# Kernel optimization log

Hardware: AMD Instinct MI355X
Metric: run time of the kernel (lower is better)

The kernel has to match this reference:

```python
import jax, jax.numpy as jnp
import numpy as np

N = 50000      # batch_num_nodes
E = 800000     # num edges (~avg degree 16)
A = 16         # num_atom_types
H = 64         # hidden dim
Z = 32         # latent dim
L_ENC = 2
L_DEC = 2
C_NORM = 16.0  # coordinate-update normalization (avg degree)


def _glorot(key, shape):
    fan = shape[-2] + shape[-1]
    return jax.random.normal(key, shape, dtype=jnp.float32) * np.float32(np.sqrt(2.0 / fan))


def _make_stack(key, n_layers, h_dim):
    # Stacked per-layer EGNN params: edge MLP (2 layers), coord head, node MLP (2 layers).
    def one(k):
        k0, k1, k2, k3, k4 = jax.random.split(k, 5)
        return (_glorot(k0, (2 * h_dim + 1, h_dim)), jnp.zeros((h_dim,), jnp.float32),
                _glorot(k1, (h_dim, h_dim)), jnp.zeros((h_dim,), jnp.float32),
                _glorot(k2, (h_dim, 1)),
                _glorot(k3, (2 * h_dim, h_dim)), jnp.zeros((h_dim,), jnp.float32),
                _glorot(k4, (h_dim, h_dim)), jnp.zeros((h_dim,), jnp.float32))
    parts = [one(k) for k in jax.random.split(key, n_layers)]
    return tuple(jnp.stack(p) for p in zip(*parts))


PARAM_NAMES = ["We1", "be1", "We2", "be2", "Wx", "Wn1", "bn1", "Wn2", "bn2"]


def setup_inputs() -> dict:
    key = jax.random.key(0)
    k = jax.random.split(key, 10)
    h = jax.random.normal(k[0], (N, A), dtype=jnp.float32)
    x = jax.random.normal(k[1], (N, 3), dtype=jnp.float32)
    edge_index = jax.random.randint(k[2], (2, E), 0, N, dtype=jnp.int32)
    inp = {"h": h, "x": x, "edge_index": edge_index,
           "W_emb": _glorot(k[3], (A, H)), "b_emb": jnp.zeros((H,), jnp.float32),
           "W_lat": _glorot(k[4], (H, Z)), "b_lat": jnp.zeros((Z,), jnp.float32),
           "W_up": _glorot(k[5], (Z, H)), "b_up": jnp.zeros((H,), jnp.float32),
           "W_out": _glorot(k[6], (H, A)), "b_out": jnp.zeros((A,), jnp.float32)}
    for n, p in zip(PARAM_NAMES, _make_stack(k[7], L_ENC, H)):
        inp["enc_" + n] = p
    for n, p in zip(PARAM_NAMES, _make_stack(k[8], L_DEC, H)):
        inp["dec_" + n] = p
    return inp


def _egnn_layer(h, x, src, dst, We1, be1, We2, be2, Wx, Wn1, bn1, Wn2, bn2):
    rel = x[src] - x[dst]                                    # [E, 3] gather
    d2 = jnp.sum(rel * rel, axis=-1, keepdims=True)          # [E, 1]
    ef = jnp.concatenate([h[src], h[dst], d2], axis=-1)      # [E, 2H+1]
    m = jax.nn.silu(jax.nn.silu(ef @ We1 + be1) @ We2 + be2)  # [E, H] per-edge message
    # equivariant coordinate update: scatter-add weighted relative vectors
    x = x + jax.ops.segment_sum(rel * (m @ Wx), dst, num_segments=N) / C_NORM
    agg = jnp.asarray(jax.ops.segment_sum(m, dst, num_segments=N))  # [N, H]
    h = h + jax.nn.silu(jnp.concatenate([h, agg], axis=-1) @ Wn1 + bn1) @ Wn2 + bn2
    return h, x


def reference(h, x, edge_index, W_emb, b_emb, W_lat, b_lat, W_up, b_up, W_out, b_out,
              enc_We1, enc_be1, enc_We2, enc_be2, enc_Wx, enc_Wn1, enc_bn1, enc_Wn2, enc_bn2,
              dec_We1, dec_be1, dec_We2, dec_be2, dec_Wx, dec_Wn1, dec_bn1, dec_Wn2, dec_bn2):
    src, dst = edge_index[0], edge_index[1]
    hh = h @ W_emb + b_emb
    for i in range(L_ENC):
        hh, x = _egnn_layer(hh, x, src, dst,
                            enc_We1[i], enc_be1[i], enc_We2[i], enc_be2[i], enc_Wx[i],
                            enc_Wn1[i], enc_bn1[i], enc_Wn2[i], enc_bn2[i])
    z = hh @ W_lat + b_lat                                   # latent [N, Z]
    hh = z @ W_up + b_up
    for i in range(L_DEC):
        hh, x = _egnn_layer(hh, x, src, dst,
                            dec_We1[i], dec_be1[i], dec_We2[i], dec_be2[i], dec_Wx[i],
                            dec_Wn1[i], dec_bn1[i], dec_Wn2[i], dec_bn2[i])
    h_rec = hh @ W_out + b_out                               # reconstructed atom-type logits
    return jnp.concatenate([h_rec, x], axis=-1)              # [N, A+3]
```

## Files before the change

kernel.cpp:

```cpp
#include <hip/hip_runtime.h>

#define NN 50000
#define NE 800000
#define MAXC 100000
#define EBLK 2048
#define SCB ((NN + 255) / 256)

__device__ __forceinline__ float silu_f(float v) {
    return v * __builtin_amdgcn_rcpf(1.f + __expf(-v));
}

typedef __bf16 bf16;
typedef bf16 v8bf __attribute__((ext_vector_type(8)));
typedef float v4f __attribute__((ext_vector_type(4)));

#define UNPACK8(dstv, ptr) { \
    float4 _a = reinterpret_cast<const float4*>(ptr)[0]; \
    float4 _b = reinterpret_cast<const float4*>(ptr)[1]; \
    dstv[0]=_a.x; dstv[1]=_a.y; dstv[2]=_a.z; dstv[3]=_a.w; \
    dstv[4]=_b.x; dstv[5]=_b.y; dstv[6]=_b.z; dstv[7]=_b.w; }

__global__ __launch_bounds__(256) void k_embed(
    const float* __restrict__ h_in, const float* __restrict__ x_in,
    const float* __restrict__ W, const float* __restrict__ b,
    float* __restrict__ h, float* __restrict__ xp)
{
    int t = blockIdx.x * 256 + threadIdx.x;
    if (t < NN * 4) { int n = t >> 2, c = t & 3; xp[t] = (c < 3) ? x_in[n * 3 + c] : 0.f; }
    int n = t >> 6, j = t & 63;
    const float* hr = h_in + n * 16;
    float acc = b[j];
#pragma unroll
    for (int k = 0; k < 16; k++) acc = fmaf(hr[k], W[k * 64 + j], acc);
    h[t] = acc;
}

__global__ __launch_bounds__(256) void k_prep_all(
    const float* __restrict__ eW1, const float* __restrict__ dW1,
    const float* __restrict__ eW2, const float* __restrict__ dW2,
    const float* __restrict__ eN1, const float* __restrict__ dN1,
    const float* __restrict__ eN2, const float* __restrict__ dN2,
    bf16* __restrict__ We1h, bf16* __restrict__ We1l,
    bf16* __restrict__ We2h, bf16* __restrict__ We2l,
    bf16* __restrict__ Wn1h, bf16* __restrict__ Wn1l,
    bf16* __restrict__ Wn2h, bf16* __restrict__ Wn2l)
{
    int t = blockIdx.x * 256 + threadIdx.x;
    const float *encW, *decW; int K, stride; bf16 *Wh, *Wl; int r;
    if (t < 32768)      { r = t;         encW = eW1; decW = dW1; K = 128; stride = 129 * 64; Wh = We1h; Wl = We1l; }
    else if (t < 49152) { r = t - 32768; encW = eW2; decW = dW2; K = 64;  stride = 64 * 64;  Wh = We2h; Wl = We2l; }
    else if (t < 81920) { r = t - 49152; encW = eN1; decW = dN1; K = 128; stride = 128 * 64; Wh = Wn1h; Wl = Wn1l; }
    else                { r = t - 81920; encW = eN2; decW = dN2; K = 64;  stride = 64 * 64;  Wh = Wn2h; Wl = Wn2l; }
    int per = K * 64;
    int li = r / per, rr = r - li * per;
    int k = rr >> 6, col = rr & 63;
    const float* Wsrc = (li < 2 ? encW : decW) + (li & 1) * stride;
    float w = Wsrc[k * 64 + col];
    bf16 hi = (bf16)w;
    int kh = k >> 5, gg = (k >> 3) & 3, b = k & 7;
    int di = li * per + (((kh * 4 + gg) * 64 + col) * 8 + b);
    Wh[di] = hi; Wl[di] = (bf16)(w - (float)hi);
}

__global__ __launch_bounds__(256) void k_zero_cnt(int* __restrict__ cnt)
{
    int t = blockIdx.x * 256 + threadIdx.x;
    if (t <= NN) cnt[t] = 0;
}

__global__ __launch_bounds__(256) void k_hist(const int* __restrict__ dst, int* __restrict__ cnt)
{
    int e = blockIdx.x * 256 + threadIdx.x;
    if (e < NE) atomicAdd(&cnt[dst[e]], 1);
}

__global__ __launch_bounds__(256) void k_blocksum(
    const int* __restrict__ cnt, int* __restrict__ bsum)
{
    int b = blockIdx.x, tid = threadIdx.x;
    int i = b * 256 + tid;
    int deg = (i < NN) ? cnt[i] : 0;
    int chk = (deg + 15) >> 4;
#pragma unroll
    for (int d = 1; d < 64; d <<= 1) { deg += __shfl_xor(deg, d); chk += __shfl_xor(chk, d); }
    __shared__ int sd[4], sc[4];
    int wv = tid >> 6;
    if ((tid & 63) == 0) { sd[wv] = deg; sc[wv] = chk; }
    __syncthreads();
    if (tid == 0) {
        bsum[b] = sd[0] + sd[1] + sd[2] + sd[3];
        bsum[SCB + b] = sc[0] + sc[1] + sc[2] + sc[3];
    }
}

__global__ __launch_bounds__(256) void k_scanbase(
    const int* __restrict__ bsum, int* __restrict__ bbase, int* __restrict__ ncptr)
{
    __shared__ int s[256], s2[256];
    int tid = threadIdx.x;
    int v  = (tid < SCB) ? bsum[tid] : 0;
    int v2 = (tid < SCB) ? bsum[SCB + tid] : 0;
    s[tid] = v; s2[tid] = v2;
    __syncthreads();
    for (int d = 1; d < 256; d <<= 1) {
        int u  = (tid >= d) ? s[tid - d] : 0;
        int u2 = (tid >= d) ? s2[tid - d] : 0;
        __syncthreads();
        s[tid] += u; s2[tid] += u2;
        __syncthreads();
    }
    if (tid < SCB) {
        bbase[tid]       = s[tid] - v;
        bbase[SCB + tid] = s2[tid] - v2;
    }
    if (tid == 255) *ncptr = s2[SCB - 1];
}

__global__ __launch_bounds__(256) void k_applyscan(
    int* __restrict__ cnt , const int* __restrict__ bbase,
    int* __restrict__ off, int* __restrict__ cur, int* __restrict__ coff)
{
    int b = blockIdx.x, tid = threadIdx.x;
    int i = b * 256 + tid;
    int deg = (i < NN) ? cnt[i] : 0;
    int chk = (deg + 15) >> 4;
    __shared__ int s[256], s2[256];
    s[tid] = deg; s2[tid] = chk;
    __syncthreads();
    for (int d = 1; d < 256; d <<= 1) {
        int u  = (tid >= d) ? s[tid - d] : 0;
        int u2 = (tid >= d) ? s2[tid - d] : 0;
        __syncthreads();
        s[tid] += u; s2[tid] += u2;
        __syncthreads();
    }
    if (i < NN) {
        int o = bbase[b] + s[tid] - deg;
        off[i] = o; cur[i] = o;
        coff[i] = bbase[SCB + b] + s2[tid] - chk;
    }
    if (i == 0) off[NN] = NE;
}

__global__ __launch_bounds__(256) void k_chunkfill(
    const int* __restrict__ off, const int* __restrict__ coff, int2* __restrict__ cpair)
{
    int n = blockIdx.x * 256 + threadIdx.x;
    if (n >= NN) return;
    int b = off[n], e = off[n + 1], co = coff[n];
    int single = ((e - b) <= 16) ? (1 << 25) : 0;
    for (int eb = b; eb < e; eb += 16) {
        int cnt = min(e - eb, 16);
        cpair[co++] = make_int2(n, eb | (cnt << 20) | single);
    }
}

__global__ __launch_bounds__(256) void k_scatter(
    const int* __restrict__ dst, const int* __restrict__ srcArr,
    int* __restrict__ cur, int* __restrict__ srcp)
{
    int e = blockIdx.x * 256 + threadIdx.x;
    if (e < NE) { int p = atomicAdd(&cur[dst[e]], 1); srcp[p] = srcArr[e]; }
}

__global__ __launch_bounds__(256) void k_pq_mfma(
    const float* __restrict__ h,
    const bf16* __restrict__ We1h, const bf16* __restrict__ We1l,
    const float* __restrict__ be1,
    float* __restrict__ P, float* __restrict__ Q,
    float* __restrict__ agg, float* __restrict__ dxb)
{
    const int wv = threadIdx.x >> 6, lane = threadIdx.x & 63;
    const int g = lane >> 4, l15 = lane & 15;
    const int n0 = (blockIdx.x * 4 + wv) * 16;
    if (n0 >= NN) return;
    const int nrow = n0 + l15;

    v8bf Ah[2], Al[2];
#pragma unroll
    for (int kh = 0; kh < 2; kh++) {
        float v[8];
        UNPACK8(v, h + nrow * 64 + kh * 32 + g * 8);
#pragma unroll
        for (int b = 0; b < 8; b++) {
            bf16 hi = (bf16)v[b];
            Ah[kh][b] = hi; Al[kh][b] = (bf16)(v[b] - (float)hi);
        }
    }

    const v8bf* Bh = reinterpret_cast<const v8bf*>(We1h);
    const v8bf* Bl = reinterpret_cast<const v8bf*>(We1l);

    float be1v[4];
#pragma unroll
    for (int nt = 0; nt < 4; nt++) be1v[nt] = be1[l15 + 16 * nt];

#pragma unroll
    for (int nt = 0; nt < 4; nt++) {
        v4f ap = {0.f,0.f,0.f,0.f}, aq = {0.f,0.f,0.f,0.f};
#pragma unroll
        for (int kh = 0; kh < 2; kh++) {
            int fiP = (kh * 4 + g) * 64 + l15 + 16 * nt;
            int fiQ = ((kh + 2) * 4 + g) * 64 + l15 + 16 * nt;
            v8bf bph = Bh[fiP], bpl = Bl[fiP];
            v8bf bqh = Bh[fiQ], bql = Bl[fiQ];
            ap = __builtin_amdgcn_mfma_f32_16x16x32_bf16(Ah[kh], bph, ap, 0, 0, 0);
            ap = __builtin_amdgcn_mfma_f32_16x16x32_bf16(Ah[kh], bpl, ap, 0, 0, 0);
            ap = __builtin_amdgcn_mfma_f32_16x16x32_bf16(Al[kh], bph, ap, 0, 0, 0);
            aq = __builtin_amdgcn_mfma_f32_16x16x32_bf16(Ah[kh], bqh, aq, 0, 0, 0);
            aq = __builtin_amdgcn_mfma_f32_16x16x32_bf16(Ah[kh], bql, aq, 0, 0, 0);
            aq = __builtin_amdgcn_mfma_f32_16x16x32_bf16(Al[kh], bqh, aq, 0, 0, 0);
        }
#pragma unroll
        for (int i = 0; i < 4; i++) {
            int ro = (n0 + g * 4 + i) * 64 + l15 + 16 * nt;
            P[ro] = ap[i] + be1v[nt];
            Q[ro] = aq[i];
            agg[ro] = 0.f;
        }
    }
    {
        int nd = lane >> 2, cc = lane & 3;
        if (cc < 3) dxb[(n0 + nd) * 3 + cc] = 0.f;
    }
}

__device__ __forceinline__ void edge_compute(
    int n, int ct, int sg,
    const float4& xn, const float4& xs,
    const float4* pw, const float4* qv4,
    const v8bf* __restrict__ BHf, const v8bf* __restrict__ BLf,
    const float (&wdv)[2][8], const float (&be2v)[4], const float (&wxv)[4],
    int g, int l15, int lane,
    float* __restrict__ agg, float* __restrict__ dxb)
{
    float rx = xs.x - xn.x, ry = xs.y - xn.y, rz = xs.z - xn.z;
    float d2 = rx * rx + ry * ry + rz * rz;
    const float* pv = reinterpret_cast<const float*>(pw);
    const float* qv = reinterpret_cast<const float*>(qv4);

    v8bf Ah[2], Al[2];
#pragma unroll
    for (int kh = 0; kh < 2; kh++) {
#pragma unroll
        for (int b = 0; b < 8; b++) {
            float m1 = silu_f(pv[kh * 8 + b] + qv[kh * 8 + b] + d2 * wdv[kh][b]);
            bf16 hi = (bf16)m1;
            Ah[kh][b] = hi;
            Al[kh][b] = (bf16)(m1 - (float)hi);
        }
    }

    v4f acc[4];
#pragma unroll
    for (int nt = 0; nt < 4; nt++) {
        v4f a = {0.f, 0.f, 0.f, 0.f};
#pragma unroll
        for (int kh = 0; kh < 2; kh++) {
            int fi = (kh * 4 + g) * 64 + l15 + 16 * nt;
            v8bf bh = BHf[fi], bl = BLf[fi];
            a = __builtin_amdgcn_mfma_f32_16x16x32_bf16(Ah[kh], bh, a, 0, 0, 0);
            a = __builtin_amdgcn_mfma_f32_16x16x32_bf16(Ah[kh], bl, a, 0, 0, 0);
            a = __builtin_amdgcn_mfma_f32_16x16x32_bf16(Al[kh], bh, a, 0, 0, 0);
        }
        acc[nt] = a;
    }

    float aggv[4] = {0.f, 0.f, 0.f, 0.f};
    float dxx = 0.f, dxy = 0.f, dxz = 0.f;
#pragma unroll
    for (int i = 0; i < 4; i++) {
        bool valid = (g * 4 + i) < ct;
        float m0 = silu_f(acc[0][i] + be2v[0]); m0 = valid ? m0 : 0.f;
        float m1 = silu_f(acc[1][i] + be2v[1]); m1 = valid ? m1 : 0.f;
        float m2 = silu_f(acc[2][i] + be2v[2]); m2 = valid ? m2 : 0.f;
        float m3 = silu_f(acc[3][i] + be2v[3]); m3 = valid ? m3 : 0.f;
        aggv[0] += m0; aggv[1] += m1; aggv[2] += m2; aggv[3] += m3;
        float pd = m0 * wxv[0] + m1 * wxv[1] + m2 * wxv[2] + m3 * wxv[3];
        pd += __shfl_xor(pd, 1); pd += __shfl_xor(pd, 2);
        pd += __shfl_xor(pd, 4); pd += __shfl_xor(pd, 8);
        float rxe = __shfl(rx, g * 4 + i);
        float rye = __shfl(ry, g * 4 + i);
        float rze = __shfl(rz, g * 4 + i);
        if (l15 == 0) { dxx += rxe * pd; dxy += rye * pd; dxz += rze * pd; }
    }

#pragma unroll
    for (int nt = 0; nt < 4; nt++) {
        aggv[nt] += __shfl_xor(aggv[nt], 16);
        aggv[nt] += __shfl_xor(aggv[nt], 32);
    }
    if (lane < 16) {
        if (sg) {
#pragma unroll
            for (int nt = 0; nt < 4; nt++) agg[n * 64 + l15 + 16 * nt] = aggv[nt];
        } else {
#pragma unroll
            for (int nt = 0; nt < 4; nt++) unsafeAtomicAdd(&agg[n * 64 + l15 + 16 * nt], aggv[nt]);
        }
    }
    dxx += __shfl_xor(dxx, 16); dxx += __shfl_xor(dxx, 32);
    dxy += __shfl_xor(dxy, 16); dxy += __shfl_xor(dxy, 32);
    dxz += __shfl_xor(dxz, 16); dxz += __shfl_xor(dxz, 32);
    if (lane == 0) {
        if (sg) {
            dxb[n * 3 + 0] = dxx; dxb[n * 3 + 1] = dxy; dxb[n * 3 + 2] = dxz;
        } else {
            unsafeAtomicAdd(&dxb[n * 3 + 0], dxx);
            unsafeAtomicAdd(&dxb[n * 3 + 1], dxy);
            unsafeAtomicAdd(&dxb[n * 3 + 2], dxz);
        }
    }
}

__global__ __launch_bounds__(256) void k_edge_pipe(
    const int* __restrict__ srcp, const int2* __restrict__ cpair, const int* __restrict__ ncptr,
    const float* __restrict__ xp,
    const float* __restrict__ P, const float* __restrict__ Q,
    const float* __restrict__ Wd,
    const bf16* __restrict__ We2h, const bf16* __restrict__ We2l,
    const float* __restrict__ be2, const float* __restrict__ Wx,
    float* __restrict__ agg, float* __restrict__ dxb)
{
    const int wv = threadIdx.x >> 6, lane = threadIdx.x & 63;
    const int g = lane >> 4, l15 = lane & 15;
    const int Wstride = EBLK * 4;
    const int NC = *ncptr;
    int c0 = blockIdx.x * 4 + wv;
    if (c0 >= NC) return;

    const float4* xp4 = reinterpret_cast<const float4*>(xp);
    const float4* Pf4 = reinterpret_cast<const float4*>(P);
    const float4* Qf4 = reinterpret_cast<const float4*>(Q);
    const v8bf* BHf = reinterpret_cast<const v8bf*>(We2h);
    const v8bf* BLf = reinterpret_cast<const v8bf*>(We2l);

    float wdv[2][8];
    UNPACK8(wdv[0], Wd + g * 8);
    UNPACK8(wdv[1], Wd + 32 + g * 8);
    float be2v[4], wxv[4];
#pragma unroll
    for (int nt = 0; nt < 4; nt++) { be2v[nt] = be2[l15 + 16 * nt]; wxv[nt] = Wx[l15 + 16 * nt]; }

    int c1 = c0 + Wstride, c2 = c1 + Wstride, c3 = c2 + Wstride;
    int2 m0 = cpair[c0];
    int2 m1 = cpair[min(c1, NC - 1)];
    int2 m2 = cpair[min(c2, NC - 1)];
    int n0 = m0.x, eb0 = m0.y & 0xFFFFF, ct0 = (m0.y >> 20) & 31, sg0 = (m0.y >> 25) & 1;
    int n1 = m1.x, eb1 = m1.y & 0xFFFFF, ct1 = (m1.y >> 20) & 31, sg1 = (m1.y >> 25) & 1;
    int s0 = srcp[eb0 + min(l15, ct0 - 1)];
    int s1 = srcp[eb1 + min(l15, ct1 - 1)];
    float4 xn0 = xp4[n0], xn1 = xp4[n1];
    float4 xs0 = xp4[s0];
    float4 pw0[4], qv0[4];
    pw0[0] = Pf4[s0 * 16 + g * 2];     pw0[1] = Pf4[s0 * 16 + g * 2 + 1];
    pw0[2] = Pf4[s0 * 16 + 8 + g * 2]; pw0[3] = Pf4[s0 * 16 + 8 + g * 2 + 1];
    qv0[0] = Qf4[n0 * 16 + g * 2];     qv0[1] = Qf4[n0 * 16 + g * 2 + 1];
    qv0[2] = Qf4[n0 * 16 + 8 + g * 2]; qv0[3] = Qf4[n0 * 16 + 8 + g * 2 + 1];

    while (true) {
        float4 xs1 = xp4[s1];
        float4 pw1[4], qv1[4];
        pw1[0] = Pf4[s1 * 16 + g * 2];     pw1[1] = Pf4[s1 * 16 + g * 2 + 1];
        pw1[2] = Pf4[s1 * 16 + 8 + g * 2]; pw1[3] = Pf4[s1 * 16 + 8 + g * 2 + 1];
        qv1[0] = Qf4[n1 * 16 + g * 2];     qv1[1] = Qf4[n1 * 16 + g * 2 + 1];
        qv1[2] = Qf4[n1 * 16 + 8 + g * 2]; qv1[3] = Qf4[n1 * 16 + 8 + g * 2 + 1];
        int n2 = m2.x, eb2 = m2.y & 0xFFFFF, ct2 = (m2.y >> 20) & 31, sg2 = (m2.y >> 25) & 1;
        int s2 = srcp[eb2 + min(l15, ct2 - 1)];
        float4 xn2 = xp4[n2];
        int2 m3 = cpair[min(c3, NC - 1)];

        edge_compute(n0, ct0, sg0, xn0, xs0, pw0, qv0,
                     BHf, BLf, wdv, be2v, wxv, g, l15, lane, agg, dxb);

        c0 = c1; c1 = c2; c2 = c3; c3 += Wstride;
        n0 = n1; ct0 = ct1; sg0 = sg1; xn0 = xn1; xs0 = xs1;
#pragma unroll
        for (int j = 0; j < 4; j++) { pw0[j] = pw1[j]; qv0[j] = qv1[j]; }
        n1 = n2; ct1 = ct2; sg1 = sg2; s1 = s2; xn1 = xn2;
        m2 = m3;
        if (c0 >= NC) break;
    }
}

__global__ __launch_bounds__(256) void k_node_mfma(
    float* __restrict__ h, float* __restrict__ xp,
    float* __restrict__ agg, const float* __restrict__ dxb,
    const bf16* __restrict__ Wn1h, const bf16* __restrict__ Wn1l, const float* __restrict__ bn1,
    const bf16* __restrict__ Wn2h, const bf16* __restrict__ Wn2l, const float* __restrict__ bn2,
    int do_pq,
    const bf16* __restrict__ We1nh, const bf16* __restrict__ We1nl, const float* __restrict__ be1n,
    float* __restrict__ P, float* __restrict__ Q, float* __restrict__ dxbz)
{
    __shared__ float sh[4][16][68];
    __shared__ float su[4][16][68];

    const int wv = threadIdx.x >> 6, lane = threadIdx.x & 63;
    const int g = lane >> 4, l15 = lane & 15;
    const int n0 = (blockIdx.x * 4 + wv) * 16;
    if (n0 >= NN) return;

    const int nrow = n0 + l15;

    v8bf Ah[4], Al[4];
#pragma unroll
    for (int kh = 0; kh < 2; kh++) {
        float v[8];
        UNPACK8(v, h + nrow * 64 + kh * 32 + g * 8);
        *reinterpret_cast<float4*>(&sh[wv][l15][kh * 32 + g * 8])     = *reinterpret_cast<const float4*>(&v[0]);
        *reinterpret_cast<float4*>(&sh[wv][l15][kh * 32 + g * 8 + 4]) = *reinterpret_cast<const float4*>(&v[4]);
#pragma unroll
        for (int b = 0; b < 8; b++) {
            bf16 hi = (bf16)v[b];
            Ah[kh][b] = hi; Al[kh][b] = (bf16)(v[b] - (float)hi);
        }
    }
#pragma unroll
    for (int kh = 0; kh < 2; kh++) {
        float v[8];
        UNPACK8(v, agg + nrow * 64 + kh * 32 + g * 8);
#pragma unroll
        for (int b = 0; b < 8; b++) {
            bf16 hi = (bf16)v[b];
            Ah[2 + kh][b] = hi; Al[2 + kh][b] = (bf16)(v[b] - (float)hi);
        }
    }

    const v8bf* B1h = reinterpret_cast<const v8bf*>(Wn1h);
    const v8bf* B1l = reinterpret_cast<const v8bf*>(Wn1l);
    const v8bf* B2h = reinterpret_cast<const v8bf*>(Wn2h);
    const v8bf* B2l = reinterpret_cast<const v8bf*>(Wn2l);

    float bn1v[4];
#pragma unroll
    for (int nt = 0; nt < 4; nt++) bn1v[nt] = bn1[l15 + 16 * nt];
#pragma unroll
    for (int nt = 0; nt < 4; nt++) {
        v4f a = {0.f, 0.f, 0.f, 0.f};
#pragma unroll
        for (int kh = 0; kh < 4; kh++) {
            int fi = (kh * 4 + g) * 64 + l15 + 16 * nt;
            v8bf bh = B1h[fi], bl = B1l[fi];
            a = __builtin_amdgcn_mfma_f32_16x16x32_bf16(Ah[kh], bh, a, 0, 0, 0);
            a = __builtin_amdgcn_mfma_f32_16x16x32_bf16(Ah[kh], bl, a, 0, 0, 0);
            a = __builtin_amdgcn_mfma_f32_16x16x32_bf16(Al[kh], bh, a, 0, 0, 0);
        }
#pragma unroll
        for (int i = 0; i < 4; i++)
            su[wv][g * 4 + i][l15 + 16 * nt] = silu_f(a[i] + bn1v[nt]);
    }
    asm volatile("s_waitcnt lgkmcnt(0)" ::: "memory");

    v8bf Uh[2], Ul[2];
#pragma unroll
    for (int kh = 0; kh < 2; kh++) {
        float v[8];
        *reinterpret_cast<float4*>(&v[0]) = *reinterpret_cast<const float4*>(&su[wv][l15][kh * 32 + g * 8]);
        *reinterpret_cast<float4*>(&v[4]) = *reinterpret_cast<const float4*>(&su[wv][l15][kh * 32 + g * 8 + 4]);
#pragma unroll
        for (int b = 0; b < 8; b++) {
            bf16 hi = (bf16)v[b];
            Uh[kh][b] = hi; Ul[kh][b] = (bf16)(v[b] - (float)hi);
        }
    }

    float bn2v[4];
#pragma unroll
    for (int nt = 0; nt < 4; nt++) bn2v[nt] = bn2[l15 + 16 * nt];
#pragma unroll
    for (int nt = 0; nt < 4; nt++) {
        v4f a = {0.f, 0.f, 0.f, 0.f};
#pragma unroll
        for (int kh = 0; kh < 2; kh++) {
            int fi = (kh * 4 + g) * 64 + l15 + 16 * nt;
            v8bf bh = B2h[fi], bl = B2l[fi];
            a = __builtin_amdgcn_mfma_f32_16x16x32_bf16(Uh[kh], bh, a, 0, 0, 0);
            a = __builtin_amdgcn_mfma_f32_16x16x32_bf16(Uh[kh], bl, a, 0, 0, 0);
            a = __builtin_amdgcn_mfma_f32_16x16x32_bf16(Ul[kh], bh, a, 0, 0, 0);
        }
#pragma unroll
        for (int i = 0; i < 4; i++) {
            float hout = sh[wv][g * 4 + i][l15 + 16 * nt] + a[i] + bn2v[nt];
            h[(n0 + g * 4 + i) * 64 + l15 + 16 * nt] = hout;
            if (do_pq) sh[wv][g * 4 + i][l15 + 16 * nt] = hout;
        }
    }

    {
        int nd = lane >> 2, cc = lane & 3;
        if (cc < 3) {
            xp[(n0 + nd) * 4 + cc] += dxb[(n0 + nd) * 3 + cc] * (1.f / 16.f);
            if (do_pq) dxbz[(n0 + nd) * 3 + cc] = 0.f;
        }
    }

    if (do_pq) {
        asm volatile("s_waitcnt lgkmcnt(0)" ::: "memory");
        v8bf Hh[2], Hl[2];
#pragma unroll
        for (int kh = 0; kh < 2; kh++) {
            float v[8];
            *reinterpret_cast<float4*>(&v[0]) = *reinterpret_cast<const float4*>(&sh[wv][l15][kh * 32 + g * 8]);
            *reinterpret_cast<float4*>(&v[4]) = *reinterpret_cast<const float4*>(&sh[wv][l15][kh * 32 + g * 8 + 4]);
#pragma unroll
            for (int b = 0; b < 8; b++) {
                bf16 hi = (bf16)v[b];
                Hh[kh][b] = hi; Hl[kh][b] = (bf16)(v[b] - (float)hi);
            }
        }
        const v8bf* Bh = reinterpret_cast<const v8bf*>(We1nh);
        const v8bf* Bl = reinterpret_cast<const v8bf*>(We1nl);
        float be1v[4];
#pragma unroll
        for (int nt = 0; nt < 4; nt++) be1v[nt] = be1n[l15 + 16 * nt];
#pragma unroll
        for (int nt = 0; nt < 4; nt++) {
            v4f ap = {0.f,0.f,0.f,0.f}, aq = {0.f,0.f,0.f,0.f};
#pragma unroll
            for (int kh = 0; kh < 2; kh++) {
                int fiP = (kh * 4 + g) * 64 + l15 + 16 * nt;
                int fiQ = ((kh + 2) * 4 + g) * 64 + l15 + 16 * nt;
                v8bf bph = Bh[fiP], bpl = Bl[fiP];
                v8bf bqh = Bh[fiQ], bql = Bl[fiQ];
                ap = __builtin_amdgcn_mfma_f32_16x16x32_bf16(Hh[kh], bph, ap, 0, 0, 0);
                ap = __builtin_amdgcn_mfma_f32_16x16x32_bf16(Hh[kh], bpl, ap, 0, 0, 0);
                ap = __builtin_amdgcn_mfma_f32_16x16x32_bf16(Hl[kh], bph, ap, 0, 0, 0);
                aq = __builtin_amdgcn_mfma_f32_16x16x32_bf16(Hh[kh], bqh, aq, 0, 0, 0);
                aq = __builtin_amdgcn_mfma_f32_16x16x32_bf16(Hh[kh], bql, aq, 0, 0, 0);
                aq = __builtin_amdgcn_mfma_f32_16x16x32_bf16(Hl[kh], bqh, aq, 0, 0, 0);
            }
#pragma unroll
            for (int i = 0; i < 4; i++) {
                int ro = (n0 + g * 4 + i) * 64 + l15 + 16 * nt;
                P[ro] = ap[i] + be1v[nt];
                Q[ro] = aq[i];
                agg[ro] = 0.f;
            }
        }
    }
}

__global__ __launch_bounds__(256) void k_latent(
    float* __restrict__ h, const float* __restrict__ Wl, const float* __restrict__ bl,
    const float* __restrict__ Wu, const float* __restrict__ bu)
{
    __shared__ float sWl[2048], sWu[2048];
    __shared__ __align__(16) float shh[4][8][64];
    __shared__ __align__(16) float sz[4][8][32];
    for (int i = threadIdx.x; i < 2048; i += 256) { sWl[i] = Wl[i]; sWu[i] = Wu[i]; }
    int wv = threadIdx.x >> 6, j = threadIdx.x & 63;
    int base = (blockIdx.x * 4 + wv) * 8;
#pragma unroll
    for (int r = 0; r < 8; r++) { int n = base + r; shh[wv][r][j] = (n < NN) ? h[n * 64 + j] : 0.f; }
    __syncthreads();
    if (j < 32) {
        float acc[8];
        float b0 = bl[j];
#pragma unroll
        for (int r = 0; r < 8; r++) acc[r] = b0;
        for (int kb = 0; kb < 16; kb++) {
            float w0 = sWl[(4 * kb + 0) * 32 + j], w1 = sWl[(4 * kb + 1) * 32 + j];
            float w2 = sWl[(4 * kb + 2) * 32 + j], w3 = sWl[(4 * kb + 3) * 32 + j];
#pragma unroll
            for (int r = 0; r < 8; r++) {
                float4 m = *reinterpret_cast<const float4*>(&shh[wv][r][4 * kb]);
                acc[r] += m.x * w0 + m.y * w1 + m.z * w2 + m.w * w3;
            }
        }
#pragma unroll
        for (int r = 0; r < 8; r++) sz[wv][r][j] = acc[r];
    }
    __syncthreads();
    float acc2[8];
    float b1 = bu[j];
#pragma unroll
    for (int r = 0; r < 8; r++) acc2[r] = b1;
    for (int kb = 0; kb < 8; kb++) {
        float w0 = sWu[(4 * kb + 0) * 64 + j], w1 = sWu[(4 * kb + 1) * 64 + j];
        float w2 = sWu[(4 * kb + 2) * 64 + j], w3 = sWu[(4 * kb + 3) * 64 + j];
#pragma unroll
        for (int r = 0; r < 8; r++) {
            float4 m = *reinterpret_cast<const float4*>(&sz[wv][r][4 * kb]);
            acc2[r] += m.x * w0 + m.y * w1 + m.z * w2 + m.w * w3;
        }
    }
#pragma unroll
    for (int r = 0; r < 8; r++) { int n = base + r; if (n < NN) h[n * 64 + j] = acc2[r]; }
}

__global__ __launch_bounds__(256) void k_out(
    const float* __restrict__ h, const float* __restrict__ xp,
    const float* __restrict__ Wo, const float* __restrict__ bo,
    float* __restrict__ out)
{
    int t = blockIdx.x * 256 + threadIdx.x;
    if (t >= NN * 19) return;
    int n = t / 19, c = t - n * 19;
    if (c < 16) {
        const float4* hr = reinterpret_cast<const float4*>(h + n * 64);
        float acc = bo[c];
#pragma unroll
        for (int kb = 0; kb < 16; kb++) {
            float4 hv = hr[kb];
            acc = fmaf(hv.x, Wo[(4 * kb + 0) * 16 + c], acc);
            acc = fmaf(hv.y, Wo[(4 * kb + 1) * 16 + c], acc);
            acc = fmaf(hv.z, Wo[(4 * kb + 2) * 16 + c], acc);
            acc = fmaf(hv.w, Wo[(4 * kb + 3) * 16 + c], acc);
        }
        out[t] = acc;
    } else {
        out[t] = xp[n * 4 + (c - 16)];
    }
}

extern "C" void kernel_launch(void* const* d_in, const int* in_sizes, int n_in,
                              void* d_out, int out_size, void* d_ws, size_t ws_size,
                              hipStream_t stream)
{
    const float* h_in  = (const float*)d_in[0];
    const float* x_in  = (const float*)d_in[1];
    const int*   ei    = (const int*)d_in[2];
    const float* W_emb = (const float*)d_in[3];
    const float* b_emb = (const float*)d_in[4];
    const float* W_lat = (const float*)d_in[5];
    const float* b_lat = (const float*)d_in[6];
    const float* W_up  = (const float*)d_in[7];
    const float* b_up  = (const float*)d_in[8];
    const float* W_out = (const float*)d_in[9];
    const float* b_out = (const float*)d_in[10];
    const float* encp[9]; const float* decp[9];
    for (int i = 0; i < 9; i++) { encp[i] = (const float*)d_in[11 + i]; decp[i] = (const float*)d_in[20 + i]; }

    const int* src = ei;
    const int* dst = ei + NE;

    float* ws  = (float*)d_ws;
    float* h   = ws;
    float* xp  = h + NN * 64;
    float* P   = xp + NN * 4;
    float* Q   = P + NN * 64;
    float* agg = Q + NN * 64;
    float* dxb = agg + NN * 64;
    int* off   = (int*)(dxb + NN * 3);
    int* cur   = off + (NN + 1);
    int* coff  = cur + (NN + 1);
    int* bsum  = coff + NN;
    int* bbase = bsum + 2 * SCB;
    int* srcp  = bbase + 2 * SCB;
    int* ncptr = srcp + NE;
    int2* cpair = (int2*)(ncptr + 2);
    bf16* We1h = (bf16*)(cpair + MAXC);
    bf16* We1l = We1h + 4 * 8192;
    bf16* We2h = We1l + 4 * 8192;
    bf16* We2l = We2h + 4 * 4096;
    bf16* Wn1h = We2l + 4 * 4096;
    bf16* Wn1l = Wn1h + 4 * 8192;
    bf16* Wn2h = Wn1l + 4 * 8192;
    bf16* Wn2l = Wn2h + 4 * 4096;

    k_zero_cnt<<<(NN + 256) / 256, 256, 0, stream>>>(cur);
    k_hist<<<NE / 256, 256, 0, stream>>>(dst, cur);
    k_blocksum<<<SCB, 256, 0, stream>>>(cur, bsum);
    k_scanbase<<<1, 256, 0, stream>>>(bsum, bbase, ncptr);
    k_applyscan<<<SCB, 256, 0, stream>>>(cur, bbase, off, cur, coff);
    k_scatter<<<NE / 256, 256, 0, stream>>>(dst, src, cur, srcp);
    k_chunkfill<<<(NN + 255) / 256, 256, 0, stream>>>(off, coff, cpair);
    k_prep_all<<<384, 256, 0, stream>>>(encp[0], decp[0], encp[2], decp[2],
                                        encp[5], decp[5], encp[7], decp[7],
                                        We1h, We1l, We2h, We2l, Wn1h, Wn1l, Wn2h, Wn2l);

    k_embed<<<(NN * 64) / 256, 256, 0, stream>>>(h_in, x_in, W_emb, b_emb, h, xp);

    const int NODE_GRID = (NN / 16 + 3) / 4;

    k_pq_mfma<<<NODE_GRID, 256, 0, stream>>>(h, We1h, We1l, encp[1], P, Q, agg, dxb);

    for (int L = 0; L < 4; ++L) {
        const float** pp = (L < 2) ? encp : decp;
        int li = (L < 2) ? L : L - 2;
        const float* We1 = pp[0] + li * 129 * 64;
        const float* be2 = pp[3] + li * 64;
        const float* Wx  = pp[4] + li * 64;
        const float* bn1 = pp[6] + li * 64;
        const float* bn2 = pp[8] + li * 64;

        k_edge_pipe<<<EBLK, 256, 0, stream>>>(srcp, cpair, ncptr,
                                              xp, P, Q, We1 + 128 * 64,
                                              We2h + L * 4096, We2l + L * 4096,
                                              be2, Wx, agg, dxb);

        int do_pq = (L == 0 || L == 2) ? 1 : 0;
        int Ln = L + 1;
        const float* be1n = do_pq ? ((Ln < 2 ? encp[1] : decp[1]) + (Ln & 1) * 64) : bn1;
        k_node_mfma<<<NODE_GRID, 256, 0, stream>>>(h, xp, agg, dxb,
                                                   Wn1h + L * 8192, Wn1l + L * 8192, bn1,
                                                   Wn2h + L * 4096, Wn2l + L * 4096, bn2,
                                                   do_pq,
                                                   We1h + (L + 1) * 8192, We1l + (L + 1) * 8192, be1n,
                                                   P, Q, dxb);

        if (L == 1) {
            k_latent<<<(NN + 31) / 32, 256, 0, stream>>>(h, W_lat, b_lat, W_up, b_up);
            k_pq_mfma<<<NODE_GRID, 256, 0, stream>>>(h, We1h + 2 * 8192, We1l + 2 * 8192,
                                                     decp[1], P, Q, agg, dxb);
        }
    }

    k_out<<<(NN * 19 + 255) / 256, 256, 0, stream>>>(h, xp, W_out, b_out, (float*)d_out);
}
```

Baseline: 667.1 us.

## Fuse latent projection into node kernel, merge chunkfill into scan, tweak edge loop

Result: faster. 627.4 us (-6.0%).

```diff
diff --git a/kernel.cpp b/kernel.cpp
--- a/kernel.cpp
+++ b/kernel.cpp
@@ -40,25 +40,45 @@
     const float* __restrict__ eW2, const float* __restrict__ dW2,
     const float* __restrict__ eN1, const float* __restrict__ dN1,
     const float* __restrict__ eN2, const float* __restrict__ dN2,
+    const float* __restrict__ Wlat, const float* __restrict__ Wup,
     bf16* __restrict__ We1h, bf16* __restrict__ We1l,
     bf16* __restrict__ We2h, bf16* __restrict__ We2l,
     bf16* __restrict__ Wn1h, bf16* __restrict__ Wn1l,
-    bf16* __restrict__ Wn2h, bf16* __restrict__ Wn2l)
+    bf16* __restrict__ Wn2h, bf16* __restrict__ Wn2l,
+    bf16* __restrict__ Wlh,  bf16* __restrict__ Wll,
+    bf16* __restrict__ Wuh,  bf16* __restrict__ Wul)
 {
     int t = blockIdx.x * 256 + threadIdx.x;
-    const float *encW, *decW; int K, stride; bf16 *Wh, *Wl; int r;
-    if (t < 32768)      { r = t;         encW = eW1; decW = dW1; K = 128; stride = 129 * 64; Wh = We1h; Wl = We1l; }
-    else if (t < 49152) { r = t - 32768; encW = eW2; decW = dW2; K = 64;  stride = 64 * 64;  Wh = We2h; Wl = We2l; }
-    else if (t < 81920) { r = t - 49152; encW = eN1; decW = dN1; K = 128; stride = 128 * 64; Wh = Wn1h; Wl = Wn1l; }
-    else                { r = t - 81920; encW = eN2; decW = dN2; K = 64;  stride = 64 * 64;  Wh = Wn2h; Wl = Wn2l; }
-    int per = K * 64;
-    int li = r / per, rr = r - li * per;
-    int k = rr >> 6, col = rr & 63;
-    const float* Wsrc = (li < 2 ? encW : decW) + (li & 1) * stride;
-    float w = Wsrc[k * 64 + col];
+    float w; int di; bf16 *Wh, *Wl;
+    if (t < 98304) {
+        const float *encW, *decW; int K, stride; int r;
+        if (t < 32768)      { r = t;         encW = eW1; decW = dW1; K = 128; stride = 129 * 64; Wh = We1h; Wl = We1l; }
+        else if (t < 49152) { r = t - 32768; encW = eW2; decW = dW2; K = 64;  stride = 64 * 64;  Wh = We2h; Wl = We2l; }
+        else if (t < 81920) { r = t - 49152; encW = eN1; decW = dN1; K = 128; stride = 128 * 64; Wh = Wn1h; Wl = Wn1l; }
+        else                { r = t - 81920; encW = eN2; decW = dN2; K = 64;  stride = 64 * 64;  Wh = Wn2h; Wl = Wn2l; }
+        int per = K * 64;
+        int li = r / per, rr = r - li * per;
+        int k = rr >> 6, col = rr & 63;
+        const float* Wsrc = (li < 2 ? encW : decW) + (li & 1) * stride;
+        w = Wsrc[k * 64 + col];
+        int kh = k >> 5, gg = (k >> 3) & 3, b = k & 7;
+        di = li * per + (((kh * 4 + gg) * 64 + col) * 8 + b);
+    } else if (t < 100352) {
+        int r = t - 98304;
+        int k = r >> 5, col = r & 31;
+        w = Wlat[k * 32 + col];
+        int kh = k >> 5, gg = (k >> 3) & 3, b = k & 7;
+        di = ((kh * 4 + gg) * 32 + col) * 8 + b;
+        Wh = Wlh; Wl = Wll;
+    } else {
+        int r = t - 100352;
+        int k = r >> 6, col = r & 63;
+        w = Wup[k * 64 + col];
+        int gg = (k >> 3) & 3, b = k & 7;
+        di = (gg * 64 + col) * 8 + b;
+        Wh = Wuh; Wl = Wul;
+    }
     bf16 hi = (bf16)w;
-    int kh = k >> 5, gg = (k >> 3) & 3, b = k & 7;
-    int di = li * per + (((kh * 4 + gg) * 64 + col) * 8 + b);
     Wh[di] = hi; Wl[di] = (bf16)(w - (float)hi);
 }
 
@@ -117,8 +137,8 @@
 }
 
 __global__ __launch_bounds__(256) void k_applyscan(
-    int* __restrict__ cnt , const int* __restrict__ bbase,
-    int* __restrict__ off, int* __restrict__ cur, int* __restrict__ coff)
+    int* __restrict__ cnt, const int* __restrict__ bbase,
+    int* __restrict__ off, int* __restrict__ cur, int2* __restrict__ cpair)
 {
     int b = blockIdx.x, tid = threadIdx.x;
     int i = b * 256 + tid;
@@ -137,22 +157,15 @@
     if (i < NN) {
         int o = bbase[b] + s[tid] - deg;
         off[i] = o; cur[i] = o;
-        coff[i] = bbase[SCB + b] + s2[tid] - chk;
+        int co = bbase[SCB + b] + s2[tid] - chk;
+        int e = o + deg;
+        int single = (deg <= 16) ? (1 << 25) : 0;
+        for (int eb = o; eb < e; eb += 16) {
+            int c = min(e - eb, 16);
+            cpair[co++] = make_int2(i, eb | (c << 20) | single);
+        }
     }
     if (i == 0) off[NN] = NE;
-}
-
-__global__ __launch_bounds__(256) void k_chunkfill(
-    const int* __restrict__ off, const int* __restrict__ coff, int2* __restrict__ cpair)
-{
-    int n = blockIdx.x * 256 + threadIdx.x;
-    if (n >= NN) return;
-    int b = off[n], e = off[n + 1], co = coff[n];
-    int single = ((e - b) <= 16) ? (1 << 25) : 0;
-    for (int eb = b; eb < e; eb += 16) {
-        int cnt = min(e - eb, 16);
-        cpair[co++] = make_int2(n, eb | (cnt << 20) | single);
-    }
 }
 
 __global__ __launch_bounds__(256) void k_scatter(
@@ -252,6 +265,7 @@
     }
 
     v4f acc[4];
+    __builtin_amdgcn_s_setprio(1);
 #pragma unroll
     for (int nt = 0; nt < 4; nt++) {
         v4f a = {0.f, 0.f, 0.f, 0.f};
@@ -265,6 +279,7 @@
         }
         acc[nt] = a;
     }
+    __builtin_amdgcn_s_setprio(0);
 
     float aggv[4] = {0.f, 0.f, 0.f, 0.f};
     float dxx = 0.f, dxy = 0.f, dxz = 0.f;
@@ -328,6 +343,7 @@
     const int NC = *ncptr;
     int c0 = blockIdx.x * 4 + wv;
     if (c0 >= NC) return;
+    const int T = (NC - c0 + Wstride - 1) / Wstride;
 
     const float4* xp4 = reinterpret_cast<const float4*>(xp);
     const float4* Pf4 = reinterpret_cast<const float4*>(P);
@@ -342,10 +358,10 @@
 #pragma unroll
     for (int nt = 0; nt < 4; nt++) { be2v[nt] = be2[l15 + 16 * nt]; wxv[nt] = Wx[l15 + 16 * nt]; }
 
-    int c1 = c0 + Wstride, c2 = c1 + Wstride, c3 = c2 + Wstride;
+    int c3 = c0 + 3 * Wstride;
     int2 m0 = cpair[c0];
-    int2 m1 = cpair[min(c1, NC - 1)];
-    int2 m2 = cpair[min(c2, NC - 1)];
+    int2 m1 = cpair[min(c0 + Wstride, NC - 1)];
+    int2 m2 = cpair[min(c0 + 2 * Wstride, NC - 1)];
     int n0 = m0.x, eb0 = m0.y & 0xFFFFF, ct0 = (m0.y >> 20) & 31, sg0 = (m0.y >> 25) & 1;
     int n1 = m1.x, eb1 = m1.y & 0xFFFFF, ct1 = (m1.y >> 20) & 31, sg1 = (m1.y >> 25) & 1;
     int s0 = srcp[eb0 + min(l15, ct0 - 1)];
@@ -358,7 +374,8 @@
     qv0[0] = Qf4[n0 * 16 + g * 2];     qv0[1] = Qf4[n0 * 16 + g * 2 + 1];
     qv0[2] = Qf4[n0 * 16 + 8 + g * 2]; qv0[3] = Qf4[n0 * 16 + 8 + g * 2 + 1];
 
-    while (true) {
+#pragma unroll 2
+    for (int t = 0; t < T; t++) {
         float4 xs1 = xp4[s1];
         float4 pw1[4], qv1[4];
         pw1[0] = Pf4[s1 * 16 + g * 2];     pw1[1] = Pf4[s1 * 16 + g * 2 + 1];
@@ -373,13 +390,12 @@
         edge_compute(n0, ct0, sg0, xn0, xs0, pw0, qv0,
                      BHf, BLf, wdv, be2v, wxv, g, l15, lane, agg, dxb);
 
-        c0 = c1; c1 = c2; c2 = c3; c3 += Wstride;
+        c3 += Wstride;
         n0 = n1; ct0 = ct1; sg0 = sg1; xn0 = xn1; xs0 = xs1;
 #pragma unroll
         for (int j = 0; j < 4; j++) { pw0[j] = pw1[j]; qv0[j] = qv1[j]; }
         n1 = n2; ct1 = ct2; sg1 = sg2; s1 = s2; xn1 = xn2;
         m2 = m3;
-        if (c0 >= NC) break;
     }
 }
 
@@ -390,7 +406,10 @@
     const bf16* __restrict__ Wn2h, const bf16* __restrict__ Wn2l, const float* __restrict__ bn2,
     int do_pq,
     const bf16* __restrict__ We1nh, const bf16* __restrict__ We1nl, const float* __restrict__ be1n,
-    float* __restrict__ P, float* __restrict__ Q, float* __restrict__ dxbz)
+    float* __restrict__ P, float* __restrict__ Q, float* __restrict__ dxbz,
+    int do_lat,
+    const bf16* __restrict__ Wlh, const bf16* __restrict__ Wll, const float* __restrict__ bl,
+    const bf16* __restrict__ Wuh, const bf16* __restrict__ Wul, const float* __restrict__ bu)
 {
     __shared__ float sh[4][16][68];
     __shared__ float su[4][16][68];
@@ -440,9 +459,9 @@
 #pragma unroll
         for (int kh = 0; kh < 4; kh++) {
             int fi = (kh * 4 + g) * 64 + l15 + 16 * nt;
-            v8bf bh = B1h[fi], bl = B1l[fi];
+            v8bf bh = B1h[fi], bl_ = B1l[fi];
             a = __builtin_amdgcn_mfma_f32_16x16x32_bf16(Ah[kh], bh, a, 0, 0, 0);
-            a = __builtin_amdgcn_mfma_f32_16x16x32_bf16(Ah[kh], bl, a, 0, 0, 0);
+            a = __builtin_amdgcn_mfma_f32_16x16x32_bf16(Ah[kh], bl_, a, 0, 0, 0);
             a = __builtin_amdgcn_mfma_f32_16x16x32_bf16(Al[kh], bh, a, 0, 0, 0);
         }
 #pragma unroll
@@ -473,16 +492,16 @@
 #pragma unroll
         for (int kh = 0; kh < 2; kh++) {
             int fi = (kh * 4 + g) * 64 + l15 + 16 * nt;
-            v8bf bh = B2h[fi], bl = B2l[fi];
+            v8bf bh = B2h[fi], bl_ = B2l[fi];
             a = __builtin_amdgcn_mfma_f32_16x16x32_bf16(Uh[kh], bh, a, 0, 0, 0);
-            a = __builtin_amdgcn_mfma_f32_16x16x32_bf16(Uh[kh], bl, a, 0, 0, 0);
+            a = __builtin_amdgcn_mfma_f32_16x16x32_bf16(Uh[kh], bl_, a, 0, 0, 0);
             a = __builtin_amdgcn_mfma_f32_16x16x32_bf16(Ul[kh], bh, a, 0, 0, 0);
         }
 #pragma unroll
         for (int i = 0; i < 4; i++) {
             float hout = sh[wv][g * 4 + i][l15 + 16 * nt] + a[i] + bn2v[nt];
-            h[(n0 + g * 4 + i) * 64 + l15 + 16 * nt] = hout;
-            if (do_pq) sh[wv][g * 4 + i][l15 + 16 * nt] = hout;
+            if (!do_lat) h[(n0 + g * 4 + i) * 64 + l15 + 16 * nt] = hout;
+            if (do_pq || do_lat) sh[wv][g * 4 + i][l15 + 16 * nt] = hout;
         }
     }
 
@@ -491,6 +510,72 @@
         if (cc < 3) {
             xp[(n0 + nd) * 4 + cc] += dxb[(n0 + nd) * 3 + cc] * (1.f / 16.f);
             if (do_pq) dxbz[(n0 + nd) * 3 + cc] = 0.f;
+        }
+    }
+
+    if (do_lat) {
+        asm volatile("s_waitcnt lgkmcnt(0)" ::: "memory");
+        v8bf Hh[2], Hl[2];
+#pragma unroll
+        for (int kh = 0; kh < 2; kh++) {
+            float v[8];
+            *reinterpret_cast<float4*>(&v[0]) = *reinterpret_cast<const float4*>(&sh[wv][l15][kh * 32 + g * 8]);
+            *reinterpret_cast<float4*>(&v[4]) = *reinterpret_cast<const float4*>(&sh[wv][l15][kh * 32 + g * 8 + 4]);
+#pragma unroll
+            for (int b = 0; b < 8; b++) {
+                bf16 hi = (bf16)v[b];
+                Hh[kh][b] = hi; Hl[kh][b] = (bf16)(v[b] - (float)hi);
+            }
+        }
+        const v8bf* BLh = reinterpret_cast<const v8bf*>(Wlh);
+        const v8bf* BLl = reinterpret_cast<const v8bf*>(Wll);
+#pragma unroll
+        for (int nt = 0; nt < 2; nt++) {
+            v4f a = {0.f, 0.f, 0.f, 0.f};
+#pragma unroll
+            for (int kh = 0; kh < 2; kh++) {
+                int fi = (kh * 4 + g) * 32 + l15 + 16 * nt;
+                v8bf bh = BLh[fi], bl_ = BLl[fi];
+                a = __builtin_amdgcn_mfma_f32_16x16x32_bf16(Hh[kh], bh, a, 0, 0, 0);
+                a = __builtin_amdgcn_mfma_f32_16x16x32_bf16(Hh[kh], bl_, a, 0, 0, 0);
+                a = __builtin_amdgcn_mfma_f32_16x16x32_bf16(Hl[kh], bh, a, 0, 0, 0);
+            }
+            float blv = bl[l15 + 16 * nt];
+#pragma unroll
+            for (int i = 0; i < 4; i++)
+                su[wv][g * 4 + i][l15 + 16 * nt] = a[i] + blv;
+        }
+        asm volatile("s_waitcnt lgkmcnt(0)" ::: "memory");
+
+        v8bf Zh, Zl;
+        {
+            float v[8];
+            *reinterpret_cast<float4*>(&v[0]) = *reinterpret_cast<const float4*>(&su[wv][l15][g * 8]);
+            *reinterpret_cast<float4*>(&v[4]) = *reinterpret_cast<const float4*>(&su[wv][l15][g * 8 + 4]);
+#pragma unroll
+            for (int b = 0; b < 8; b++) {
+                bf16 hi = (bf16)v[b];
+                Zh[b] = hi; Zl[b] = (bf16)(v[b] - (float)hi);
+            }
+        }
+        const v8bf* BUh = reinterpret_cast<const v8bf*>(Wuh);
+        const v8bf* BUl = reinterpret_cast<const v8bf*>(Wul);
+        asm volatile("s_waitcnt lgkmcnt(0)" ::: "memory");
+#pragma unroll
+        for (int nt = 0; nt < 4; nt++) {
+            v4f a = {0.f, 0.f, 0.f, 0.f};
+            int fi = g * 64 + l15 + 16 * nt;
+            v8bf bh = BUh[fi], bl_ = BUl[fi];
+            a = __builtin_amdgcn_mfma_f32_16x16x32_bf16(Zh, bh, a, 0, 0, 0);
+            a = __builtin_amdgcn_mfma_f32_16x16x32_bf16(Zh, bl_, a, 0, 0, 0);
+            a = __builtin_amdgcn_mfma_f32_16x16x32_bf16(Zl, bh, a, 0, 0, 0);
+            float buv = bu[l15 + 16 * nt];
+#pragma unroll
+            for (int i = 0; i < 4; i++) {
+                float hout = a[i] + buv;
+                h[(n0 + g * 4 + i) * 64 + l15 + 16 * nt] = hout;
+                sh[wv][g * 4 + i][l15 + 16 * nt] = hout;
+            }
         }
     }
 
@@ -538,54 +623,6 @@
             }
         }
     }
-}
-
-__global__ __launch_bounds__(256) void k_latent(
-    float* __restrict__ h, const float* __restrict__ Wl, const float* __restrict__ bl,
-    const float* __restrict__ Wu, const float* __restrict__ bu)
-{
-    __shared__ float sWl[2048], sWu[2048];
-    __shared__ __align__(16) float shh[4][8][64];
-    __shared__ __align__(16) float sz[4][8][32];
-    for (int i = threadIdx.x; i < 2048; i += 256) { sWl[i] = Wl[i]; sWu[i] = Wu[i]; }
-    int wv = threadIdx.x >> 6, j = threadIdx.x & 63;
-    int base = (blockIdx.x * 4 + wv) * 8;
-#pragma unroll
-    for (int r = 0; r < 8; r++) { int n = base + r; shh[wv][r][j] = (n < NN) ? h[n * 64 + j] : 0.f; }
-    __syncthreads();
-    if (j < 32) {
-        float acc[8];
-        float b0 = bl[j];
-#pragma unroll
-        for (int r = 0; r < 8; r++) acc[r] = b0;
-        for (int kb = 0; kb < 16; kb++) {
-            float w0 = sWl[(4 * kb + 0) * 32 + j], w1 = sWl[(4 * kb + 1) * 32 + j];
-            float w2 = sWl[(4 * kb + 2) * 32 + j], w3 = sWl[(4 * kb + 3) * 32 + j];
-#pragma unroll
-            for (int r = 0; r < 8; r++) {
-                float4 m = *reinterpret_cast<const float4*>(&shh[wv][r][4 * kb]);
-                acc[r] += m.x * w0 + m.y * w1 + m.z * w2 + m.w * w3;
-            }
-        }
-#pragma unroll
-        for (int r = 0; r < 8; r++) sz[wv][r][j] = acc[r];
-    }
-    __syncthreads();
-    float acc2[8];
-    float b1 = bu[j];
-#pragma unroll
-    for (int r = 0; r < 8; r++) acc2[r] = b1;
-    for (int kb = 0; kb < 8; kb++) {
-        float w0 = sWu[(4 * kb + 0) * 64 + j], w1 = sWu[(4 * kb + 1) * 64 + j];
-        float w2 = sWu[(4 * kb + 2) * 64 + j], w3 = sWu[(4 * kb + 3) * 64 + j];
-#pragma unroll
-        for (int r = 0; r < 8; r++) {
-            float4 m = *reinterpret_cast<const float4*>(&sz[wv][r][4 * kb]);
-            acc2[r] += m.x * w0 + m.y * w1 + m.z * w2 + m.w * w3;
-        }
-    }
-#pragma unroll
-    for (int r = 0; r < 8; r++) { int n = base + r; if (n < NN) h[n * 64 + j] = acc2[r]; }
 }
 
 __global__ __launch_bounds__(256) void k_out(
@@ -643,8 +680,7 @@
     float* dxb = agg + NN * 64;
     int* off   = (int*)(dxb + NN * 3);
     int* cur   = off + (NN + 1);
-    int* coff  = cur + (NN + 1);
-    int* bsum  = coff + NN;
+    int* bsum  = cur + (NN + 1);
     int* bbase = bsum + 2 * SCB;
     int* srcp  = bbase + 2 * SCB;
     int* ncptr = srcp + NE;
@@ -657,17 +693,22 @@
     bf16* Wn1l = Wn1h + 4 * 8192;
     bf16* Wn2h = Wn1l + 4 * 8192;
     bf16* Wn2l = Wn2h + 4 * 4096;
+    bf16* Wlh  = Wn2l + 4 * 4096;
+    bf16* Wll  = Wlh + 2048;
+    bf16* Wuh  = Wll + 2048;
+    bf16* Wul  = Wuh + 2048;
 
     k_zero_cnt<<<(NN + 256) / 256, 256, 0, stream>>>(cur);
     k_hist<<<NE / 256, 256, 0, stream>>>(dst, cur);
     k_blocksum<<<SCB, 256, 0, stream>>>(cur, bsum);
     k_scanbase<<<1, 256, 0, stream>>>(bsum, bbase, ncptr);
-    k_applyscan<<<SCB, 256, 0, stream>>>(cur, bbase, off, cur, coff);
+    k_applyscan<<<SCB, 256, 0, stream>>>(cur, bbase, off, cur, cpair);
     k_scatter<<<NE / 256, 256, 0, stream>>>(dst, src, cur, srcp);
-    k_chunkfill<<<(NN + 255) / 256, 256, 0, stream>>>(off, coff, cpair);
-    k_prep_all<<<384, 256, 0, stream>>>(encp[0], decp[0], encp[2], decp[2],
+    k_prep_all<<<400, 256, 0, stream>>>(encp[0], decp[0], encp[2], decp[2],
                                         encp[5], decp[5], encp[7], decp[7],
-                                        We1h, We1l, We2h, We2l, Wn1h, Wn1l, Wn2h, Wn2l);
+                                        W_lat, W_up,
+                                        We1h, We1l, We2h, We2l, Wn1h, Wn1l, Wn2h, Wn2l,
+                                        Wlh, Wll, Wuh, Wul);
 
     k_embed<<<(NN * 64) / 256, 256, 0, stream>>>(h_in, x_in, W_emb, b_emb, h, xp);
 
@@ -689,21 +730,19 @@
                                               We2h + L * 4096, We2l + L * 4096,
                                               be2, Wx, agg, dxb);
 
-        int do_pq = (L == 0 || L == 2) ? 1 : 0;
+        int do_pq = (L < 3) ? 1 : 0;
+        int do_lat = (L == 1) ? 1 : 0;
         int Ln = L + 1;
-        const float* be1n = do_pq ? ((Ln < 2 ? encp[1] : decp[1]) + (Ln & 1) * 64) : bn1;
+        const float* be1n = bn1;
+        if (do_pq) be1n = (Ln < 2 ? encp[1] : decp[1]) + ((Ln < 2 ? Ln : Ln - 2)) * 64;
+
         k_node_mfma<<<NODE_GRID, 256, 0, stream>>>(h, xp, agg, dxb,
                                                    Wn1h + L * 8192, Wn1l + L * 8192, bn1,
                                                    Wn2h + L * 4096, Wn2l + L * 4096, bn2,
                                                    do_pq,
-                                                   We1h + (L + 1) * 8192, We1l + (L + 1) * 8192, be1n,
-                                                   P, Q, dxb);
-
-        if (L == 1) {
-            k_latent<<<(NN + 31) / 32, 256, 0, stream>>>(h, W_lat, b_lat, W_up, b_up);
-            k_pq_mfma<<<NODE_GRID, 256, 0, stream>>>(h, We1h + 2 * 8192, We1l + 2 * 8192,
-                                                     decp[1], P, Q, agg, dxb);
-        }
+                                                   We1h + Ln * 8192, We1l + Ln * 8192, be1n,
+                                                   P, Q, dxb,
+                                                   do_lat, Wlh, Wll, b_lat, Wuh, Wul, b_up);
     }
 
     k_out<<<(NN * 19 + 255) / 256, 256, 0, stream>>>(h, xp, W_out, b_out, (float*)d_out);
```
